# Kernel optimization log

Hardware: AMD Instinct MI355X
Metric: run time of the kernel (lower is better)

The kernel has to match this reference:

```python
import math
import jax, jax.numpy as jnp
import numpy as np

B, M, L, H = 8, 2048, 2048, 1024


def setup_inputs() -> dict:
    key = jax.random.key(0)
    k1, k2, k3, k4 = jax.random.split(key, 4)
    return {
        "query": jax.random.normal(k1, (B, M, H), dtype=jnp.float32),
        "key": jax.random.normal(k2, (B, L, H), dtype=jnp.float32),
        "value": jax.random.normal(k3, (B, L, H), dtype=jnp.float32),
        "key_pe": jax.random.normal(k4, (1, H, L), dtype=jnp.float32),
        "hidden_size": H,
    }


def reference(query, key, value, key_pe, hidden_size):
    # content scores: [B, M, L]
    attn_cont = jnp.einsum("bmh,blh->bml", query, key)
    # relative-position scores: [B, M, H] @ [1, H, L] -> [B, M, L]
    attn_pos = jnp.matmul(query, key_pe)
    # NOTE: the original module computes softmax(attn)+dropout but then
    # (as written) multiplies VALUE by the raw content scores, not the
    # softmaxed attention. We reproduce that math faithfully; the softmax
    # is dead code w.r.t. the output (kept here for documentation, DCE'd by jit).
    attn = jax.nn.softmax((attn_cont + attn_pos) / math.sqrt(hidden_size), axis=-1)  # noqa: F841
    # dropout: identity in eval mode (and unused for the output anyway)
    out = jnp.matmul(attn_cont, value)  # [B, M, H]
    return out
```

## Files before the change

### kernel.cpp

```cpp
#include <hip/hip_runtime.h>
#include <hip/hip_bf16.h>


typedef __bf16 bf16x8 __attribute__((ext_vector_type(8)));
typedef float f32x4 __attribute__((ext_vector_type(4)));
typedef unsigned short u16_t;

#define GLD_LDS16(g, l)                                                        \
  __builtin_amdgcn_global_load_lds(                                            \
      (const __attribute__((address_space(1))) void*)(g),                      \
      (__attribute__((address_space(3))) void*)(l), 16, 0, 0)

static __device__ inline u16_t f2b(float x) {
  __hip_bfloat16 h = __float2bfloat16(x);
  u16_t u;
  __builtin_memcpy(&u, &h, 2);
  return u;
}
static __device__ inline unsigned pack2(float a, float b) {
  return (unsigned)f2b(a) | ((unsigned)f2b(b) << 16);
}
static __device__ inline float b2f(u16_t u) {
  unsigned v = (unsigned)u << 16;
  float f;
  __builtin_memcpy(&f, &v, 4);
  return f;
}

__global__ __launch_bounds__(256) void transpose_kv(
    const float* __restrict__ Kin, const float* __restrict__ Vin,
    u16_t* __restrict__ Kt, u16_t* __restrict__ Vt, int L, int Hd) {
  __shared__ unsigned tile[64 * 33];
  const int bz = blockIdx.z;
  const float* in = (bz < 8) ? Kin : Vin;
  u16_t* out = (bz < 8) ? Kt : Vt;
  const int batch = bz & 7;
  in  += (size_t)batch * (size_t)L * Hd;
  out += (size_t)batch * (size_t)L * Hd;
  const int h0 = blockIdx.x * 64;
  const int l0 = blockIdx.y * 64;

  const int h4 = (threadIdx.x & 15) * 4;
  const int lp0 = threadIdx.x >> 4;
#pragma unroll
  for (int it = 0; it < 2; ++it) {
    const int lp = lp0 + 16 * it;
    const int l = 2 * lp;
    const float4 f0 = *(const float4*)(in + (size_t)(l0 + l) * Hd + h0 + h4);
    const float4 f1 = *(const float4*)(in + (size_t)(l0 + l + 1) * Hd + h0 + h4);
    tile[(h4 + 0) * 33 + lp] = pack2(f0.x, f1.x);
    tile[(h4 + 1) * 33 + lp] = pack2(f0.y, f1.y);
    tile[(h4 + 2) * 33 + lp] = pack2(f0.z, f1.z);
    tile[(h4 + 3) * 33 + lp] = pack2(f0.w, f1.w);
  }
  __syncthreads();

  const int h = threadIdx.x >> 2;
  const int half = threadIdx.x & 3;
  unsigned u[8];
#pragma unroll
  for (int j = 0; j < 8; ++j) u[j] = tile[h * 33 + 8 * half + j];
  u16_t* dst = out + (size_t)(h0 + h) * L + l0 + 16 * half;
  *(uint4*)(dst)     = *(const uint4*)(u);
  *(uint4*)(dst + 8) = *(const uint4*)(u + 4);
}

static __device__ inline void store_c(float* p, float v) { *p = v; }
static __device__ inline void store_c(u16_t* p, float v) { *p = f2b(v); }

template <typename OutT>
static __device__ inline void gemm_bt_body(
    const u16_t* __restrict__ A, const u16_t* __restrict__ Bt,
    OutT* __restrict__ C, int N, int K, int ldA, int ldB,
    long sA, long sB, long sC, int tile_shift, long sCsplit) {
  __shared__ __align__(16) u16_t As[128 * 64];
  __shared__ __align__(16) u16_t Bs[128 * 64];

  const int batch = blockIdx.x & 7;
  const unsigned u = blockIdx.x >> 3;
  const int kh = (int)(u >> tile_shift);
  const unsigned t = u & ((1u << tile_shift) - 1u);
  const int m0 = (int)(t >> 3) * 128;
  const int n0 = (int)(t & 7) * 128;

  A  += (size_t)batch * (size_t)sA + (size_t)kh * (size_t)K;
  Bt += (size_t)batch * (size_t)sB + (size_t)kh * (size_t)K;
  C  += (size_t)batch * (size_t)sC + (size_t)kh * (size_t)sCsplit;

  const int tid = threadIdx.x;
  const int lane = tid & 63;
  const int w  = tid >> 6;
  const int wm = w & 1;
  const int wn = w >> 1;
  const int s  = lane & 15;
  const int q  = lane >> 4;

  const u16_t* gA[4];
  const u16_t* gB[4];
  u16_t* lA[4];
  u16_t* lB[4];
#pragma unroll
  for (int j = 0; j < 4; ++j) {
    const int i = tid + 256 * j;
    const int row = i >> 3;
    const int gchunk = (i & 7) ^ (row & 7);
    gA[j] = A  + (size_t)(m0 + row) * ldA + gchunk * 8;
    gB[j] = Bt + (size_t)(n0 + row) * ldB + gchunk * 8;
    lA[j] = As + i * 8;
    lB[j] = Bs + i * 8;
  }

  f32x4 acc[4][4];
#pragma unroll
  for (int r = 0; r < 4; ++r)
#pragma unroll
    for (int c = 0; c < 4; ++c) acc[r][c] = (f32x4){0.f, 0.f, 0.f, 0.f};

  const int s7 = s & 7;

  for (int k0 = 0; k0 < K; k0 += 64) {
#pragma unroll
    for (int j = 0; j < 4; ++j) {
      GLD_LDS16(gA[j] + k0, lA[j]);
      GLD_LDS16(gB[j] + k0, lB[j]);
    }
    __syncthreads();

#pragma unroll
    for (int kk = 0; kk < 2; ++kk) {
      const int slot = (kk * 4 + q) ^ s7;
      bf16x8 af[4], bfr[4];
#pragma unroll
      for (int r = 0; r < 4; ++r)
        af[r] = *(const bf16x8*)(As + (64 * wm + 16 * r + s) * 64 + slot * 8);
#pragma unroll
      for (int c = 0; c < 4; ++c)
        bfr[c] = *(const bf16x8*)(Bs + (64 * wn + 16 * c + s) * 64 + slot * 8);
#pragma unroll
      for (int r = 0; r < 4; ++r)
#pragma unroll
        for (int c = 0; c < 4; ++c)
          acc[r][c] = __builtin_amdgcn_mfma_f32_16x16x32_bf16(af[r], bfr[c],
                                                              acc[r][c], 0, 0, 0);
    }
    __syncthreads();
  }

#pragma unroll
  for (int r = 0; r < 4; ++r) {
#pragma unroll
    for (int c = 0; c < 4; ++c) {
      const int col = n0 + 64 * wn + 16 * c + s;
#pragma unroll
      for (int e = 0; e < 4; ++e) {
        const int row = m0 + 64 * wm + 16 * r + q * 4 + e;
        store_c(&C[(size_t)row * N + col], acc[r][c][e]);
      }
    }
  }
}

__global__ __launch_bounds__(256) void gemm1_kv(
    const u16_t* __restrict__ Vt, const u16_t* __restrict__ Kt,
    u16_t* __restrict__ W0, int N, int K, int ld, long sA, long sB, long sC,
    long sCsplit) {
  gemm_bt_body<u16_t>(Vt, Kt, W0, N, K, ld, ld, sA, sB, sC, 6, sCsplit);
}

__global__ __launch_bounds__(256) void gemm2_qw(
    const u16_t* __restrict__ Qb, const u16_t* __restrict__ Wb,
    float* __restrict__ C, int N, int K, long sA, long sB, long sC) {
  gemm_bt_body<float>(Qb, Wb, C, N, K, K, K, sA, sB, sC, 7, 0);
}

__global__ __launch_bounds__(256) void qcvt_wsum(
    const float* __restrict__ Q, const u16_t* __restrict__ W0,
    const u16_t* __restrict__ W1, u16_t* __restrict__ Qb,
    u16_t* __restrict__ Wb, size_t nQbatch, size_t nWbatch) {
  const int batch = blockIdx.y;
  if (blockIdx.z == 0) {
    const size_t base = (size_t)batch * nQbatch +
                        (size_t)blockIdx.x * 4096 + threadIdx.x * 16;
    const float* src = Q + base;
    u16_t* dst = Qb + base;
#pragma unroll
    for (int half = 0; half < 2; ++half) {
      const float4 a = *(const float4*)(src + half * 8);
      const float4 b = *(const float4*)(src + half * 8 + 4);
      unsigned o[4] = {pack2(a.x, a.y), pack2(a.z, a.w),
                       pack2(b.x, b.y), pack2(b.z, b.w)};
      *(uint4*)(dst + half * 8) = *(const uint4*)o;
    }
  } else {
    const size_t base = (size_t)batch * nWbatch +
                        (size_t)blockIdx.x * 2048 + threadIdx.x * 8;
    const uint4 u0 = *(const uint4*)(W0 + base);
    const uint4 u1 = *(const uint4*)(W1 + base);
    const u16_t* p0 = (const u16_t*)&u0;
    const u16_t* p1 = (const u16_t*)&u1;
    u16_t o[8];
#pragma unroll
    for (int j = 0; j < 8; ++j) o[j] = f2b(b2f(p0[j]) + b2f(p1[j]));
    *(uint4*)(Wb + base) = *(const uint4*)o;
  }
}

extern "C" void kernel_launch(void* const* d_in, const int* in_sizes, int n_in,
                              void* d_out, int out_size, void* d_ws, size_t ws_size,
                              hipStream_t stream) {
  const int B = 8, M = 2048, L = 2048, H = 1024;

  const float* q = (const float*)d_in[0];
  const float* k = (const float*)d_in[1];
  const float* v = (const float*)d_in[2];

  const size_t nKt = (size_t)B * H * L;
  const size_t nW  = (size_t)B * H * H;
  const size_t need = (2 * nKt + 2 * nW) * sizeof(u16_t);
  if (ws_size < need) return;

  u16_t* Kt = (u16_t*)d_ws;
  u16_t* Vt = Kt + nKt;
  u16_t* W0 = Vt + nKt;
  u16_t* W1 = W0 + nW;
  u16_t* Qb = Kt;
  u16_t* Wb = Vt;

  dim3 tb(256);

  transpose_kv<<<dim3(H / 64, L / 64, 2 * B), tb, 0, stream>>>(k, v, Kt, Vt, L, H);

  gemm1_kv<<<dim3(B * 64 * 2), tb, 0, stream>>>(
      Vt, Kt, W0, H, L / 2, L, (long)H * L, (long)H * L, (long)H * H,
      (long)B * H * H);

  qcvt_wsum<<<dim3(512, B, 2), tb, 0, stream>>>(
      q, W0, W1, Qb, Wb, (size_t)M * H, (size_t)H * H);

  gemm2_qw<<<dim3(B * 128), tb, 0, stream>>>(
      Qb, Wb, (float*)d_out, H, H, (long)M * H, (long)H * H, (long)M * H);
}
```

Baseline: 316.0 us.

## Pad transposed K/V row stride and enlarge transpose tiles to 64x512

The transposed bf16 K and V buffers get a padded leading dimension (L+16) so the GEMM's strided global-to-LDS loads avoid power-of-two stride conflicts across channels. The transpose kernel now processes 64x512 tiles per block, batching its global loads for more memory-level parallelism and writing 16-byte rows per lane. The qcvt_wsum branches are swapped so W-sum blocks come first in z order. The cost is a larger LDS tile (about 66KB), which lowers transpose occupancy, plus a slightly larger workspace.

```diff
diff --git a/kernel.cpp b/kernel.cpp
--- a/kernel.cpp
+++ b/kernel.cpp
@@ -29,40 +29,52 @@
 
 __global__ __launch_bounds__(256) void transpose_kv(
     const float* __restrict__ Kin, const float* __restrict__ Vin,
-    u16_t* __restrict__ Kt, u16_t* __restrict__ Vt, int L, int Hd) {
-  __shared__ unsigned tile[64 * 33];
+    u16_t* __restrict__ Kt, u16_t* __restrict__ Vt, int L, int Hd, int ldT) {
+  __shared__ unsigned tile[64][260];
   const int bz = blockIdx.z;
   const float* in = (bz < 8) ? Kin : Vin;
   u16_t* out = (bz < 8) ? Kt : Vt;
   const int batch = bz & 7;
-  in  += (size_t)batch * (size_t)L * Hd;
-  out += (size_t)batch * (size_t)L * Hd;
+  in += (size_t)batch * (size_t)L * Hd;
+  out += (size_t)batch * (size_t)Hd * ldT;
   const int h0 = blockIdx.x * 64;
-  const int l0 = blockIdx.y * 64;
-
-  const int h4 = (threadIdx.x & 15) * 4;
-  const int lp0 = threadIdx.x >> 4;
-#pragma unroll
-  for (int it = 0; it < 2; ++it) {
-    const int lp = lp0 + 16 * it;
-    const int l = 2 * lp;
-    const float4 f0 = *(const float4*)(in + (size_t)(l0 + l) * Hd + h0 + h4);
-    const float4 f1 = *(const float4*)(in + (size_t)(l0 + l + 1) * Hd + h0 + h4);
-    tile[(h4 + 0) * 33 + lp] = pack2(f0.x, f1.x);
-    tile[(h4 + 1) * 33 + lp] = pack2(f0.y, f1.y);
-    tile[(h4 + 2) * 33 + lp] = pack2(f0.z, f1.z);
-    tile[(h4 + 3) * 33 + lp] = pack2(f0.w, f1.w);
+  const int l0 = blockIdx.y * 512;
+
+  const int tid = threadIdx.x;
+  const int h4 = (tid & 15) * 4;
+  const int lp0 = tid >> 4;
+
+#pragma unroll
+  for (int g = 0; g < 4; ++g) {
+    float4 r0[4], r1[4];
+#pragma unroll
+    for (int it = 0; it < 4; ++it) {
+      const int lp = lp0 + 16 * (4 * g + it);
+      const int l = l0 + 2 * lp;
+      r0[it] = *(const float4*)(in + (size_t)l * Hd + h0 + h4);
+      r1[it] = *(const float4*)(in + (size_t)(l + 1) * Hd + h0 + h4);
+    }
+#pragma unroll
+    for (int it = 0; it < 4; ++it) {
+      const int lp = lp0 + 16 * (4 * g + it);
+      tile[h4 + 0][lp] = pack2(r0[it].x, r1[it].x);
+      tile[h4 + 1][lp] = pack2(r0[it].y, r1[it].y);
+      tile[h4 + 2][lp] = pack2(r0[it].z, r1[it].z);
+      tile[h4 + 3][lp] = pack2(r0[it].w, r1[it].w);
+    }
   }
   __syncthreads();
 
-  const int h = threadIdx.x >> 2;
-  const int half = threadIdx.x & 3;
-  unsigned u[8];
-#pragma unroll
-  for (int j = 0; j < 8; ++j) u[j] = tile[h * 33 + 8 * half + j];
-  u16_t* dst = out + (size_t)(h0 + h) * L + l0 + 16 * half;
-  *(uint4*)(dst)     = *(const uint4*)(u);
-  *(uint4*)(dst + 8) = *(const uint4*)(u + 4);
+  const int wv = tid >> 6;
+  const int lane = tid & 63;
+#pragma unroll
+  for (int r = 0; r < 16; ++r) {
+    const int h = wv * 16 + r;
+    unsigned u[4];
+#pragma unroll
+    for (int j = 0; j < 4; ++j) u[j] = tile[h][4 * lane + j];
+    *(uint4*)(out + (size_t)(h0 + h) * ldT + l0 + lane * 8) = *(const uint4*)u;
+  }
 }
 
 static __device__ inline void store_c(float* p, float v) { *p = v; }
@@ -179,19 +191,6 @@
     u16_t* __restrict__ Wb, size_t nQbatch, size_t nWbatch) {
   const int batch = blockIdx.y;
   if (blockIdx.z == 0) {
-    const size_t base = (size_t)batch * nQbatch +
-                        (size_t)blockIdx.x * 4096 + threadIdx.x * 16;
-    const float* src = Q + base;
-    u16_t* dst = Qb + base;
-#pragma unroll
-    for (int half = 0; half < 2; ++half) {
-      const float4 a = *(const float4*)(src + half * 8);
-      const float4 b = *(const float4*)(src + half * 8 + 4);
-      unsigned o[4] = {pack2(a.x, a.y), pack2(a.z, a.w),
-                       pack2(b.x, b.y), pack2(b.z, b.w)};
-      *(uint4*)(dst + half * 8) = *(const uint4*)o;
-    }
-  } else {
     const size_t base = (size_t)batch * nWbatch +
                         (size_t)blockIdx.x * 2048 + threadIdx.x * 8;
     const uint4 u0 = *(const uint4*)(W0 + base);
@@ -202,6 +201,19 @@
 #pragma unroll
     for (int j = 0; j < 8; ++j) o[j] = f2b(b2f(p0[j]) + b2f(p1[j]));
     *(uint4*)(Wb + base) = *(const uint4*)o;
+  } else {
+    const size_t base = (size_t)batch * nQbatch +
+                        (size_t)blockIdx.x * 4096 + threadIdx.x * 16;
+    const float* src = Q + base;
+    u16_t* dst = Qb + base;
+#pragma unroll
+    for (int half = 0; half < 2; ++half) {
+      const float4 a = *(const float4*)(src + half * 8);
+      const float4 b = *(const float4*)(src + half * 8 + 4);
+      unsigned o[4] = {pack2(a.x, a.y), pack2(a.z, a.w),
+                       pack2(b.x, b.y), pack2(b.z, b.w)};
+      *(uint4*)(dst + half * 8) = *(const uint4*)o;
+    }
   }
 }
 
@@ -209,29 +221,33 @@
                               void* d_out, int out_size, void* d_ws, size_t ws_size,
                               hipStream_t stream) {
   const int B = 8, M = 2048, L = 2048, H = 1024;
+  const int ldT = L + 16;
 
   const float* q = (const float*)d_in[0];
   const float* k = (const float*)d_in[1];
   const float* v = (const float*)d_in[2];
 
-  const size_t nKt = (size_t)B * H * L;
-  const size_t nW  = (size_t)B * H * H;
-  const size_t need = (2 * nKt + 2 * nW) * sizeof(u16_t);
+  const size_t nKtP = (size_t)B * H * ldT;
+  const size_t nW   = (size_t)B * H * H;
+  const size_t nQ   = (size_t)B * M * H;
+  const size_t need = (2 * nKtP + 2 * nW) * sizeof(u16_t);
   if (ws_size < need) return;
 
   u16_t* Kt = (u16_t*)d_ws;
-  u16_t* Vt = Kt + nKt;
-  u16_t* W0 = Vt + nKt;
+  u16_t* Vt = Kt + nKtP;
+  u16_t* W0 = Vt + nKtP;
   u16_t* W1 = W0 + nW;
   u16_t* Qb = Kt;
   u16_t* Wb = Vt;
+  (void)nQ;
 
   dim3 tb(256);
 
-  transpose_kv<<<dim3(H / 64, L / 64, 2 * B), tb, 0, stream>>>(k, v, Kt, Vt, L, H);
+  transpose_kv<<<dim3(H / 64, L / 512, 16), tb, 0, stream>>>(k, v, Kt, Vt, L, H,
+                                                             ldT);
 
   gemm1_kv<<<dim3(B * 64 * 2), tb, 0, stream>>>(
-      Vt, Kt, W0, H, L / 2, L, (long)H * L, (long)H * L, (long)H * H,
+      Vt, Kt, W0, H, L / 2, ldT, (long)H * ldT, (long)H * ldT, (long)H * H,
       (long)B * H * H);
 
   qcvt_wsum<<<dim3(512, B, 2), tb, 0, stream>>>(
```

Result: slower. 330.4 us (+4.5%).
